# Kernel optimization log

Measured on AMD Instinct MI355X. Metric: run time of the kernel, lower is better.

Reference implementation:

```python
import jax, jax.numpy as jnp
import numpy as np

D_MODEL = 1024
NHEAD = 16
HEAD_DIM = D_MODEL // NHEAD


def setup_inputs() -> dict:
    key = jax.random.key(0)
    ks = jax.random.split(key, 7)
    B, S = 4, 2048
    scale = 1.0 / np.sqrt(D_MODEL)
    x = jax.random.normal(ks[0], (B, S, D_MODEL), dtype=jnp.float32)
    Wq = jax.random.normal(ks[1], (D_MODEL, D_MODEL), dtype=jnp.float32) * scale
    Wk = jax.random.normal(ks[2], (D_MODEL, D_MODEL), dtype=jnp.float32) * scale
    Wv = jax.random.normal(ks[3], (D_MODEL, D_MODEL), dtype=jnp.float32) * scale
    bq = jax.random.normal(ks[4], (D_MODEL,), dtype=jnp.float32) * 0.01
    bk = jax.random.normal(ks[5], (D_MODEL,), dtype=jnp.float32) * 0.01
    bv = jax.random.normal(ks[6], (D_MODEL,), dtype=jnp.float32) * 0.01
    return {"x": x, "Wq": Wq, "bq": bq, "Wk": Wk, "bk": bk, "Wv": Wv, "bv": bv}


def reference(x, Wq, bq, Wk, bk, Wv, bv):
    B, S, _ = x.shape
    # Linear projections (torch Linear: x @ W.T + b; weights here are already [in, out])
    q = x @ Wq + bq
    k = x @ Wk + bk
    v = x @ Wv + bv
    # [B, S, H, Dh] -> [B, H, S, Dh]
    q = q.reshape(B, S, NHEAD, HEAD_DIM).transpose(0, 2, 1, 3)
    k = k.reshape(B, S, NHEAD, HEAD_DIM).transpose(0, 2, 1, 3)
    v = v.reshape(B, S, NHEAD, HEAD_DIM).transpose(0, 2, 1, 3)
    # NOTE: original scales by sqrt(d_model), not sqrt(head_dim)
    scores = jnp.einsum("bhqd,bhkd->bhqk", q, k) / np.sqrt(D_MODEL).astype(np.float32)
    attn = jax.nn.softmax(scores, axis=-1)  # dropout is identity at eval
    out = jnp.einsum("bhqk,bhkd->bhqd", attn, v)
    out = out.transpose(0, 2, 1, 3).reshape(B, S, D_MODEL)
    return out
```

## Files before the change

kernel.cpp:

```cpp
#include <hip/hip_runtime.h>
#include <cstdint>
#include <cstddef>

#define SEQ 2048
#define BATCH 4
#define KVB 64
#define NT (SEQ / KVB)

typedef __attribute__((ext_vector_type(8))) unsigned short u16x8;
typedef __attribute__((ext_vector_type(8))) __bf16 bf16x8;
typedef __attribute__((ext_vector_type(4))) float f32x4;
typedef __attribute__((ext_vector_type(4))) unsigned short u16x4;

#if defined(__has_builtin)
#if __has_builtin(__builtin_amdgcn_exp2f)
#define EXP2(x) __builtin_amdgcn_exp2f(x)
#else
#define EXP2(x) exp2f(x)
#endif
#else
#define EXP2(x) exp2f(x)
#endif

static __device__ __forceinline__ unsigned short f2bf(float f) {
  unsigned u = __builtin_bit_cast(unsigned, f);
  u += 0x7fffu + ((u >> 16) & 1u);
  return (unsigned short)(u >> 16);
}

static __device__ __forceinline__ f32x4 mfma16(u16x8 a, u16x8 b, f32x4 c) {
  return __builtin_amdgcn_mfma_f32_16x16x32_bf16(
      __builtin_bit_cast(bf16x8, a), __builtin_bit_cast(bf16x8, b), c, 0, 0, 0);
}

static __device__ __forceinline__ f32x4 mfma16b(u16x8 a, bf16x8 b, f32x4 c) {
  return __builtin_amdgcn_mfma_f32_16x16x32_bf16(
      __builtin_bit_cast(bf16x8, a), b, c, 0, 0, 0);
}

static __device__ __forceinline__ void gl_lds16(const void* g, void* l) {
  __builtin_amdgcn_global_load_lds(
      (const __attribute__((address_space(1))) void*)g,
      (__attribute__((address_space(3))) void*)l, 16, 0, 0);
}

__global__ __launch_bounds__(256) void k_conv_x(const float* __restrict__ x,
                                                unsigned short* __restrict__ xb) {
  int i = (blockIdx.x * 256 + threadIdx.x) * 8;
  f32x4 a = *reinterpret_cast<const f32x4*>(x + i);
  f32x4 b = *reinterpret_cast<const f32x4*>(x + i + 4);
  u16x8 v;
  v[0] = f2bf(a[0]); v[1] = f2bf(a[1]); v[2] = f2bf(a[2]); v[3] = f2bf(a[3]);
  v[4] = f2bf(b[0]); v[5] = f2bf(b[1]); v[6] = f2bf(b[2]); v[7] = f2bf(b[3]);
  *reinterpret_cast<u16x8*>(xb + i) = v;
}

__global__ __launch_bounds__(256) void k_conv_w(const float* __restrict__ Wq,
                                                const float* __restrict__ Wk,
                                                const float* __restrict__ Wv,
                                                unsigned short* __restrict__ wt) {
  const float* W = (blockIdx.z == 0) ? Wq : (blockIdx.z == 1) ? Wk : Wv;
  unsigned short* dst = wt + (size_t)blockIdx.z * 1024 * 1024;
  __shared__ float tile[32][33];
  int n0 = blockIdx.x * 32, k0 = blockIdx.y * 32;
  int tx = threadIdx.x, ty = threadIdx.y;
#pragma unroll
  for (int i = 0; i < 4; i++) {
    int k = ty + i * 8;
    tile[k][tx] = W[(size_t)(k0 + k) * 1024 + n0 + tx];
  }
  __syncthreads();
#pragma unroll
  for (int i = 0; i < 4; i++) {
    int n = ty + i * 8;
    dst[(size_t)(n0 + n) * 1024 + k0 + tx] = f2bf(tile[tx][n]);
  }
}

__global__ __launch_bounds__(256) void k_qkv_gemm(
    const unsigned short* __restrict__ xb, const unsigned short* __restrict__ wt,
    const float* __restrict__ bq, const float* __restrict__ bk,
    const float* __restrict__ bv,
    unsigned short* __restrict__ qb, unsigned short* __restrict__ kb,
    unsigned short* __restrict__ vt) {
  __shared__ unsigned short Ah[3][128 * 32];
  __shared__ unsigned short Bh[3][128 * 32];
  const int tid = threadIdx.x;
  const int lane = tid & 63, wid = tid >> 6;
  const int ln = lane & 15, g = lane >> 4;
  const int wr = wid >> 1, wc = wid & 1;
  const int dd = blockIdx.x;
  const int xcd = dd & 7, j = dd >> 3;
  const int z = j >> 6, kk = j & 63;
  const int m0 = (((kk >> 3) << 3) | xcd) * 128;
  const int n0 = (kk & 7) * 128;
  const unsigned short* Bt = wt + (size_t)z * 1024 * 1024;

  f32x4 acc[4][4];
#pragma unroll
  for (int i = 0; i < 4; i++)
#pragma unroll
    for (int jj = 0; jj < 4; jj++) acc[i][jj] = f32x4{0.f, 0.f, 0.f, 0.f};

  const int rA0 = tid >> 2, cA0 = tid & 3;
  const int swA = (cA0 ^ ((rA0 >> 1) & 3)) << 3;
  const int rA1 = rA0 + 64;

  const unsigned short* gA0 = xb + (size_t)(m0 + rA0) * 1024 + swA;
  const unsigned short* gA1 = xb + (size_t)(m0 + rA1) * 1024 + swA;
  const unsigned short* gB0 = Bt + (size_t)(n0 + rA0) * 1024 + swA;
  const unsigned short* gB1 = Bt + (size_t)(n0 + rA1) * 1024 + swA;

#define GSTAGE(bb, k0)                                          \
  do {                                                          \
    gl_lds16(gA0 + (k0), &Ah[bb][wid * 512]);                   \
    gl_lds16(gA1 + (k0), &Ah[bb][2048 + wid * 512]);            \
    gl_lds16(gB0 + (k0), &Bh[bb][wid * 512]);                   \
    gl_lds16(gB1 + (k0), &Bh[bb][2048 + wid * 512]);            \
  } while (0)

  const int fsw = (g ^ ((ln >> 1) & 3)) << 3;

#define GCOMPUTE(bb)                                                       \
  do {                                                                     \
    u16x8 af[4], bfv[4];                                                   \
    _Pragma("unroll") for (int mi = 0; mi < 4; mi++)                       \
      af[mi] = *reinterpret_cast<const u16x8*>(                            \
          &Ah[bb][(wr * 64 + mi * 16 + ln) * 32 + fsw]);                   \
    _Pragma("unroll") for (int ni = 0; ni < 4; ni++)                       \
      bfv[ni] = *reinterpret_cast<const u16x8*>(                           \
          &Bh[bb][(wc * 64 + ni * 16 + ln) * 32 + fsw]);                   \
    __builtin_amdgcn_s_setprio(1);                                         \
    _Pragma("unroll") for (int mi = 0; mi < 4; mi++)                       \
    _Pragma("unroll") for (int ni = 0; ni < 4; ni++)                       \
      acc[mi][ni] = mfma16(af[mi], bfv[ni], acc[mi][ni]);                  \
    __builtin_amdgcn_s_setprio(0);                                         \
  } while (0)

  GSTAGE(0, 0);
  GSTAGE(1, 32);
  asm volatile("s_waitcnt vmcnt(4)" ::: "memory");
  __builtin_amdgcn_s_barrier();

  for (int t = 0; t < 30; t++) {
    GCOMPUTE(t % 3);
    GSTAGE((t + 2) % 3, (t + 2) * 32);
    asm volatile("s_waitcnt vmcnt(4)" ::: "memory");
    __builtin_amdgcn_s_barrier();
  }
  GCOMPUTE(0);
  asm volatile("s_waitcnt vmcnt(0)" ::: "memory");
  __builtin_amdgcn_s_barrier();
  GCOMPUTE(1);

  const float* bias = (z == 0) ? bq : (z == 1) ? bk : bv;
#pragma unroll
  for (int ni = 0; ni < 4; ni++) {
    int n = n0 + wc * 64 + ni * 16 + ln;
    float bb = bias[n];
    int h = n >> 6, d = n & 63;
#pragma unroll
    for (int mi = 0; mi < 4; mi++) {
      int mb = m0 + wr * 64 + mi * 16 + 4 * g;
      int b = mb >> 11, s = mb & 2047;
      if (z == 2) {
        u16x4 pv;
#pragma unroll
        for (int i = 0; i < 4; i++) pv[i] = f2bf(acc[mi][ni][i] + bb);
        int s4 = s >> 2;
        int u = s4 & 7, blk = s4 >> 3;
        int nu = ((u & 3) << 1) | (u >> 2);
        int sp = ((blk << 3) | nu) << 2;
        *reinterpret_cast<u16x4*>(
            &vt[((size_t)((b * 16 + h) * 64 + d)) * 2048 + sp]) = pv;
      } else {
        unsigned short* dst = (z == 0) ? qb : kb;
        float sc = (z == 0) ? 0.0450842200f : 1.0f;
#pragma unroll
        for (int i = 0; i < 4; i++) {
          dst[((size_t)((b * 16 + h) * 2048) + (s + i)) * 64 + d] =
              f2bf((acc[mi][ni][i] + bb) * sc);
        }
      }
    }
  }
#undef GSTAGE
#undef GCOMPUTE
}

__global__ __launch_bounds__(512) void k_attn(
    const unsigned short* __restrict__ qb, const unsigned short* __restrict__ kb,
    const unsigned short* __restrict__ vt, float* __restrict__ out) {
  __shared__ unsigned short Kl[2][KVB * 64];
  __shared__ unsigned short Vl[2][64 * KVB];
  const int tid = threadIdx.x;
  const int lane = tid & 63, wid = tid >> 6;
  const int ln = lane & 15, g = lane >> 4;
  const int flat = blockIdx.x;
  const int bh = flat & 63, qidx = flat >> 6;
  const int b = bh >> 4, h = bh & 15;
  const int q0 = qidx * 256 + wid * 32;
  const unsigned short* Qp = qb + (size_t)bh * SEQ * 64;
  const unsigned short* Kp = kb + (size_t)bh * SEQ * 64;
  const unsigned short* Vp = vt + (size_t)bh * 64 * SEQ;

  const int kr0 = tid >> 3;
  const int psw = ((tid & 7) ^ (kr0 & 7)) << 3;
  const unsigned short* srcK0 = Kp + (size_t)kr0 * 64 + psw;
  const unsigned short* srcV0 = Vp + (size_t)kr0 * SEQ + psw;

#define STAGE(bb, tt)                                                     \
  do {                                                                    \
    gl_lds16(srcK0 + (size_t)(tt) * (KVB * 64), &Kl[bb][wid * 512]);      \
    gl_lds16(srcV0 + (size_t)(tt) * KVB, &Vl[bb][wid * 512]);             \
  } while (0)

  u16x8 qf[2][2];
#pragma unroll
  for (int qt = 0; qt < 2; qt++)
#pragma unroll
    for (int dc = 0; dc < 2; dc++)
      qf[qt][dc] = *reinterpret_cast<const u16x8*>(
          &Qp[(size_t)(q0 + qt * 16 + ln) * 64 + dc * 32 + g * 8]);

  f32x4 o[4][2];
#pragma unroll
  for (int dt = 0; dt < 4; dt++)
#pragma unroll
    for (int qt = 0; qt < 2; qt++) o[dt][qt] = f32x4{0.f, 0.f, 0.f, 0.f};
  f32x4 lsum[2] = {f32x4{0.f, 0.f, 0.f, 0.f}, f32x4{0.f, 0.f, 0.f, 0.f}};

  u16x8 ones;
#pragma unroll
  for (int i = 0; i < 8; i++) ones[i] = 0x3F80;

  const int lm = ln & 7;
  const int ksw0 = (g ^ lm) << 3;
  const int ksw1 = ((4 + g) ^ lm) << 3;
  const int vsw0 = (g ^ lm) << 3;
  const int vsw1 = ((4 + g) ^ lm) << 3;

  int buf = 0;
  STAGE(0, 0);
  __syncthreads();

  for (int t = 0; t < NT; t++) {
    if (t + 1 < NT) STAGE(buf ^ 1, t + 1);

    const unsigned short* Kb = Kl[buf];
    const unsigned short* Vb = Vl[buf];

    u16x8 kf[4][2];
#pragma unroll
    for (int kt = 0; kt < 4; kt++) {
      int rb = (kt * 16 + ln) * 64;
      kf[kt][0] = *reinterpret_cast<const u16x8*>(&Kb[rb + ksw0]);
      kf[kt][1] = *reinterpret_cast<const u16x8*>(&Kb[rb + ksw1]);
    }

    f32x4 st[2][4];
    __builtin_amdgcn_s_setprio(1);
#pragma unroll
    for (int qt = 0; qt < 2; qt++)
#pragma unroll
      for (int kt = 0; kt < 4; kt++) {
        f32x4 c = f32x4{0.f, 0.f, 0.f, 0.f};
        c = mfma16(kf[kt][0], qf[qt][0], c);
        c = mfma16(kf[kt][1], qf[qt][1], c);
        st[qt][kt] = c;
      }
    __builtin_amdgcn_s_setprio(0);

#pragma unroll
    for (int qt = 0; qt < 2; qt++)
#pragma unroll
      for (int kt = 0; kt < 4; kt++)
#pragma unroll
        for (int i = 0; i < 4; i++)
          st[qt][kt][i] = EXP2(st[qt][kt][i]);

    bf16x8 pb[2][2];
#pragma unroll
    for (int qt = 0; qt < 2; qt++)
#pragma unroll
      for (int ks = 0; ks < 2; ks++)
#pragma unroll
        for (int i = 0; i < 4; i++) {
          pb[qt][ks][i] = (__bf16)st[qt][2 * ks][i];
          pb[qt][ks][4 + i] = (__bf16)st[qt][2 * ks + 1][i];
        }

    __builtin_amdgcn_s_setprio(1);
#pragma unroll
    for (int dt = 0; dt < 4; dt++) {
      int rb = (dt * 16 + ln) * 64;
      u16x8 vf0 = *reinterpret_cast<const u16x8*>(&Vb[rb + vsw0]);
      o[dt][0] = mfma16b(vf0, pb[0][0], o[dt][0]);
      o[dt][1] = mfma16b(vf0, pb[1][0], o[dt][1]);
      u16x8 vf1 = *reinterpret_cast<const u16x8*>(&Vb[rb + vsw1]);
      o[dt][0] = mfma16b(vf1, pb[0][1], o[dt][0]);
      o[dt][1] = mfma16b(vf1, pb[1][1], o[dt][1]);
    }
#pragma unroll
    for (int ks = 0; ks < 2; ks++) {
      lsum[0] = mfma16b(ones, pb[0][ks], lsum[0]);
      lsum[1] = mfma16b(ones, pb[1][ks], lsum[1]);
    }
    __builtin_amdgcn_s_setprio(0);

    __syncthreads();
    buf ^= 1;
  }

  float inv[2] = {1.f / lsum[0][0], 1.f / lsum[1][0]};

#pragma unroll
  for (int qt = 0; qt < 2; qt++) {
    int q = q0 + qt * 16 + ln;
#pragma unroll
    for (int dt = 0; dt < 4; dt++) {
      f32x4 r;
#pragma unroll
      for (int i = 0; i < 4; i++) r[i] = o[dt][qt][i] * inv[qt];
      *reinterpret_cast<f32x4*>(
          &out[((size_t)(b * SEQ + q)) * 1024 + h * 64 + dt * 16 + 4 * g]) = r;
    }
  }
#undef STAGE
}

extern "C" void kernel_launch(void* const* d_in, const int* in_sizes, int n_in,
                              void* d_out, int out_size, void* d_ws, size_t ws_size,
                              hipStream_t stream) {
  (void)in_sizes; (void)n_in; (void)out_size;
  const float* x  = (const float*)d_in[0];
  const float* Wq = (const float*)d_in[1];
  const float* bq = (const float*)d_in[2];
  const float* Wk = (const float*)d_in[3];
  const float* bk = (const float*)d_in[4];
  const float* Wv = (const float*)d_in[5];
  const float* bv = (const float*)d_in[6];
  float* out = (float*)d_out;

  char* ws = (char*)d_ws;
  if (ws_size < 73400320u) return;
  unsigned short* xb    = (unsigned short*)(ws);
  unsigned short* wt    = (unsigned short*)(ws + 16777216);
  unsigned short* qbuf  = (unsigned short*)(ws + 23068672);
  unsigned short* kbuf  = (unsigned short*)(ws + 39845888);
  unsigned short* vtbuf = (unsigned short*)(ws + 56623104);

  k_conv_x<<<4096, 256, 0, stream>>>(x, xb);
  k_conv_w<<<dim3(32, 32, 3), dim3(32, 8), 0, stream>>>(Wq, Wk, Wv, wt);
  k_qkv_gemm<<<dim3(1536), 256, 0, stream>>>(xb, wt, bq, bk, bv,
                                             qbuf, kbuf, vtbuf);
  k_attn<<<dim3(512), dim3(512), 0, stream>>>(qbuf, kbuf, vtbuf, out);
}
```

Baseline: 151.6 us.

## Triple-buffer attention K/V tiles and issue GEMM loads before compute

The attention kernel moves from double to triple buffering of K/V tiles in shared memory. It issues the load for tile t+2 before computing tile t, using explicit vmcnt waits and raw barriers in place of __syncthreads. The projection GEMM loop likewise issues the next stage's global loads before the MFMA compute instead of after. The goal is to hide global-load latency behind compute, at the cost of more LDS per block, which may reduce occupancy, and a dependence on the vmcnt counts being right.

New measurement: 165.9 us. 1.09x slower.

```diff
diff --git a/kernel.cpp b/kernel.cpp
--- a/kernel.cpp
+++ b/kernel.cpp
@@ -143,8 +143,8 @@
   __builtin_amdgcn_s_barrier();
 
   for (int t = 0; t < 30; t++) {
+    GSTAGE((t + 2) % 3, (t + 2) * 32);
     GCOMPUTE(t % 3);
-    GSTAGE((t + 2) % 3, (t + 2) * 32);
     asm volatile("s_waitcnt vmcnt(4)" ::: "memory");
     __builtin_amdgcn_s_barrier();
   }
@@ -191,8 +191,8 @@
 __global__ __launch_bounds__(512) void k_attn(
     const unsigned short* __restrict__ qb, const unsigned short* __restrict__ kb,
     const unsigned short* __restrict__ vt, float* __restrict__ out) {
-  __shared__ unsigned short Kl[2][KVB * 64];
-  __shared__ unsigned short Vl[2][64 * KVB];
+  __shared__ unsigned short Kl[3][KVB * 64];
+  __shared__ unsigned short Vl[3][64 * KVB];
   const int tid = threadIdx.x;
   const int lane = tid & 63, wid = tid >> 6;
   const int ln = lane & 15, g = lane >> 4;
@@ -240,77 +240,69 @@
   const int vsw0 = (g ^ lm) << 3;
   const int vsw1 = ((4 + g) ^ lm) << 3;
 
-  int buf = 0;
+#define ACOMPUTE(bi)                                                          \
+  do {                                                                        \
+    const unsigned short* Kb = Kl[bi];                                        \
+    const unsigned short* Vb = Vl[bi];                                        \
+    u16x8 kf[4][2];                                                           \
+    _Pragma("unroll") for (int kt = 0; kt < 4; kt++) {                        \
+      int rb = (kt * 16 + ln) * 64;                                           \
+      kf[kt][0] = *reinterpret_cast<const u16x8*>(&Kb[rb + ksw0]);            \
+      kf[kt][1] = *reinterpret_cast<const u16x8*>(&Kb[rb + ksw1]);            \
+    }                                                                         \
+    f32x4 st[2][4];                                                           \
+    __builtin_amdgcn_s_setprio(1);                                            \
+    _Pragma("unroll") for (int qt = 0; qt < 2; qt++)                          \
+    _Pragma("unroll") for (int kt = 0; kt < 4; kt++) {                        \
+      f32x4 c = f32x4{0.f, 0.f, 0.f, 0.f};                                    \
+      c = mfma16(kf[kt][0], qf[qt][0], c);                                    \
+      c = mfma16(kf[kt][1], qf[qt][1], c);                                    \
+      st[qt][kt] = c;                                                         \
+    }                                                                         \
+    __builtin_amdgcn_s_setprio(0);                                            \
+    _Pragma("unroll") for (int qt = 0; qt < 2; qt++)                          \
+    _Pragma("unroll") for (int kt = 0; kt < 4; kt++)                          \
+    _Pragma("unroll") for (int i = 0; i < 4; i++)                             \
+      st[qt][kt][i] = EXP2(st[qt][kt][i]);                                    \
+    bf16x8 pb[2][2];                                                          \
+    _Pragma("unroll") for (int qt = 0; qt < 2; qt++)                          \
+    _Pragma("unroll") for (int ks = 0; ks < 2; ks++)                          \
+    _Pragma("unroll") for (int i = 0; i < 4; i++) {                           \
+      pb[qt][ks][i] = (__bf16)st[qt][2 * ks][i];                              \
+      pb[qt][ks][4 + i] = (__bf16)st[qt][2 * ks + 1][i];                      \
+    }                                                                         \
+    __builtin_amdgcn_s_setprio(1);                                            \
+    _Pragma("unroll") for (int dt = 0; dt < 4; dt++) {                        \
+      int rb = (dt * 16 + ln) * 64;                                           \
+      u16x8 vf0 = *reinterpret_cast<const u16x8*>(&Vb[rb + vsw0]);            \
+      o[dt][0] = mfma16b(vf0, pb[0][0], o[dt][0]);                            \
+      o[dt][1] = mfma16b(vf0, pb[1][0], o[dt][1]);                            \
+      u16x8 vf1 = *reinterpret_cast<const u16x8*>(&Vb[rb + vsw1]);            \
+      o[dt][0] = mfma16b(vf1, pb[0][1], o[dt][0]);                            \
+      o[dt][1] = mfma16b(vf1, pb[1][1], o[dt][1]);                            \
+    }                                                                         \
+    _Pragma("unroll") for (int ks = 0; ks < 2; ks++) {                        \
+      lsum[0] = mfma16b(ones, pb[0][ks], lsum[0]);                            \
+      lsum[1] = mfma16b(ones, pb[1][ks], lsum[1]);                            \
+    }                                                                         \
+    __builtin_amdgcn_s_setprio(0);                                            \
+  } while (0)
+
   STAGE(0, 0);
-  __syncthreads();
-
-  for (int t = 0; t < NT; t++) {
-    if (t + 1 < NT) STAGE(buf ^ 1, t + 1);
-
-    const unsigned short* Kb = Kl[buf];
-    const unsigned short* Vb = Vl[buf];
-
-    u16x8 kf[4][2];
-#pragma unroll
-    for (int kt = 0; kt < 4; kt++) {
-      int rb = (kt * 16 + ln) * 64;
-      kf[kt][0] = *reinterpret_cast<const u16x8*>(&Kb[rb + ksw0]);
-      kf[kt][1] = *reinterpret_cast<const u16x8*>(&Kb[rb + ksw1]);
-    }
-
-    f32x4 st[2][4];
-    __builtin_amdgcn_s_setprio(1);
-#pragma unroll
-    for (int qt = 0; qt < 2; qt++)
-#pragma unroll
-      for (int kt = 0; kt < 4; kt++) {
-        f32x4 c = f32x4{0.f, 0.f, 0.f, 0.f};
-        c = mfma16(kf[kt][0], qf[qt][0], c);
-        c = mfma16(kf[kt][1], qf[qt][1], c);
-        st[qt][kt] = c;
-      }
-    __builtin_amdgcn_s_setprio(0);
-
-#pragma unroll
-    for (int qt = 0; qt < 2; qt++)
-#pragma unroll
-      for (int kt = 0; kt < 4; kt++)
-#pragma unroll
-        for (int i = 0; i < 4; i++)
-          st[qt][kt][i] = EXP2(st[qt][kt][i]);
-
-    bf16x8 pb[2][2];
-#pragma unroll
-    for (int qt = 0; qt < 2; qt++)
-#pragma unroll
-      for (int ks = 0; ks < 2; ks++)
-#pragma unroll
-        for (int i = 0; i < 4; i++) {
-          pb[qt][ks][i] = (__bf16)st[qt][2 * ks][i];
-          pb[qt][ks][4 + i] = (__bf16)st[qt][2 * ks + 1][i];
-        }
-
-    __builtin_amdgcn_s_setprio(1);
-#pragma unroll
-    for (int dt = 0; dt < 4; dt++) {
-      int rb = (dt * 16 + ln) * 64;
-      u16x8 vf0 = *reinterpret_cast<const u16x8*>(&Vb[rb + vsw0]);
-      o[dt][0] = mfma16b(vf0, pb[0][0], o[dt][0]);
-      o[dt][1] = mfma16b(vf0, pb[1][0], o[dt][1]);
-      u16x8 vf1 = *reinterpret_cast<const u16x8*>(&Vb[rb + vsw1]);
-      o[dt][0] = mfma16b(vf1, pb[0][1], o[dt][0]);
-      o[dt][1] = mfma16b(vf1, pb[1][1], o[dt][1]);
-    }
-#pragma unroll
-    for (int ks = 0; ks < 2; ks++) {
-      lsum[0] = mfma16b(ones, pb[0][ks], lsum[0]);
-      lsum[1] = mfma16b(ones, pb[1][ks], lsum[1]);
-    }
-    __builtin_amdgcn_s_setprio(0);
-
-    __syncthreads();
-    buf ^= 1;
-  }
+  STAGE(1, 1);
+  asm volatile("s_waitcnt vmcnt(2)" ::: "memory");
+  __builtin_amdgcn_s_barrier();
+
+  for (int t = 0; t < NT - 2; t++) {
+    STAGE((t + 2) % 3, t + 2);
+    ACOMPUTE(t % 3);
+    asm volatile("s_waitcnt vmcnt(2)" ::: "memory");
+    __builtin_amdgcn_s_barrier();
+  }
+  ACOMPUTE((NT - 2) % 3);
+  asm volatile("s_waitcnt vmcnt(0)" ::: "memory");
+  __builtin_amdgcn_s_barrier();
+  ACOMPUTE((NT - 1) % 3);
 
   float inv[2] = {1.f / lsum[0][0], 1.f / lsum[1][0]};
 
@@ -327,6 +319,7 @@
     }
   }
 #undef STAGE
+#undef ACOMPUTE
 }
 
 extern "C" void kernel_launch(void* const* d_in, const int* in_sizes, int n_in,
```
